# Performance work log

Measured on AMD Instinct MI355X. Metric: run time of the kernel, lower is better.

The kernel has to match this reference:

```python
import jax, jax.numpy as jnp
import numpy as np
import math

B, S, D, H, DFF = 2, 2048, 1024, 16, 4096
DK = D // H
LN_EPS = 1e-5


def setup_inputs() -> dict:
    key = jax.random.key(0)
    ks = jax.random.split(key, 16)
    s = 0.02
    inp = {
        "x": jax.random.normal(ks[0], (B, S, D), jnp.float32),
        "enc": jax.random.normal(ks[1], (B, S, D), jnp.float32),
        # causal mask for self-attention, full mask for cross-attention
        "tgt_mask": jnp.tril(jnp.ones((S, S), jnp.int32))[None, None, :, :],
        "src_mask": jnp.ones((1, 1, 1, S), jnp.int32),
        # self-attention projections (stored [in, out]; no bias)
        "sa_wq": jax.random.normal(ks[2], (D, D), jnp.float32) * s,
        "sa_wk": jax.random.normal(ks[3], (D, D), jnp.float32) * s,
        "sa_wv": jax.random.normal(ks[4], (D, D), jnp.float32) * s,
        "sa_wo": jax.random.normal(ks[5], (D, D), jnp.float32) * s,
        # cross-attention projections
        "ca_wq": jax.random.normal(ks[6], (D, D), jnp.float32) * s,
        "ca_wk": jax.random.normal(ks[7], (D, D), jnp.float32) * s,
        "ca_wv": jax.random.normal(ks[8], (D, D), jnp.float32) * s,
        "ca_wo": jax.random.normal(ks[9], (D, D), jnp.float32) * s,
        # feed-forward
        "ff_w1": jax.random.normal(ks[10], (D, DFF), jnp.float32) * s,
        "ff_b1": jnp.zeros((DFF,), jnp.float32),
        "ff_w2": jax.random.normal(ks[11], (DFF, D), jnp.float32) * s,
        "ff_b2": jnp.zeros((D,), jnp.float32),
        # layernorms (post-norm residuals)
        "ln1_g": jnp.ones((D,), jnp.float32), "ln1_b": jnp.zeros((D,), jnp.float32),
        "ln2_g": jnp.ones((D,), jnp.float32), "ln2_b": jnp.zeros((D,), jnp.float32),
        "ln3_g": jnp.ones((D,), jnp.float32), "ln3_b": jnp.zeros((D,), jnp.float32),
    }
    return inp


def _layernorm(x, g, b):
    mu = jnp.mean(x, axis=-1, keepdims=True)
    var = jnp.var(x, axis=-1, keepdims=True)
    return (x - mu) * jax.lax.rsqrt(var + LN_EPS) * g + b


def _mha(xq, xk, xv, wq, wk, wv, wo, mask):
    b, sq, d = xq.shape
    sk = xk.shape[1]
    Q = (xq @ wq).reshape(b, sq, H, DK).transpose(0, 2, 1, 3)  # [b,h,sq,dk]
    K = (xk @ wk).reshape(b, sk, H, DK).transpose(0, 2, 1, 3)
    V = (xv @ wv).reshape(b, sk, H, DK).transpose(0, 2, 1, 3)
    scores = jnp.einsum("bhqd,bhkd->bhqk", Q, K) / math.sqrt(DK)
    scores = jnp.where(mask == 0, -jnp.inf, scores)
    attn = jax.nn.softmax(scores, axis=-1)
    out = jnp.einsum("bhqk,bhkd->bhqd", attn, V)
    out = out.transpose(0, 2, 1, 3).reshape(b, sq, d)
    return out @ wo


def reference(x, enc, tgt_mask, src_mask,
              sa_wq, sa_wk, sa_wv, sa_wo,
              ca_wq, ca_wk, ca_wv, ca_wo,
              ff_w1, ff_b1, ff_w2, ff_b2,
              ln1_g, ln1_b, ln2_g, ln2_b, ln3_g, ln3_b):
    # self-attention + post-norm residual (dropout = 0)
    sa = _mha(x, x, x, sa_wq, sa_wk, sa_wv, sa_wo, tgt_mask)
    x = _layernorm(x + sa, ln1_g, ln1_b)
    # cross-attention + post-norm residual
    ca = _mha(x, enc, enc, ca_wq, ca_wk, ca_wv, ca_wo, src_mask)
    x = _layernorm(x + ca, ln2_g, ln2_b)
    # feed-forward + post-norm residual
    ff = jax.nn.relu(x @ ff_w1 + ff_b1) @ ff_w2 + ff_b2
    x = _layernorm(x + ff, ln3_g, ln3_b)
    return x
```

## Files before the change

kernel.cpp:

```cpp
#include <hip/hip_runtime.h>
#include <hip/hip_bf16.h>
#include <math.h>

#define Bc 2
#define Sc 2048
#define Dc 1024
#define Hc 16
#define DKc 64
#define DFFc 4096
#define Mrows (Bc * Sc)
#define LN_EPS 1e-5f

typedef __attribute__((ext_vector_type(8))) short short8;
typedef __attribute__((ext_vector_type(4))) float f32x4;
typedef unsigned short ushort_t;

__device__ __forceinline__ float bf2f(unsigned short u) {
  union { unsigned int i; float f; } v;
  v.i = ((unsigned int)u) << 16;
  return v.f;
}
__device__ __forceinline__ unsigned short f2bf(float f) {
  union { float f; unsigned int i; } v;
  v.f = f;
  unsigned int r = v.i + 0x7fffu + ((v.i >> 16) & 1u);
  return (unsigned short)(r >> 16);
}

__global__ __launch_bounds__(256) void cast_bf16_kernel(
    const float* __restrict__ in, ushort_t* __restrict__ out) {
  const int i = blockIdx.x * 256 + threadIdx.x;
  float4 v = reinterpret_cast<const float4*>(in)[i];
  ushort4 o;
  o.x = f2bf(v.x); o.y = f2bf(v.y); o.z = f2bf(v.z); o.w = f2bf(v.w);
  reinterpret_cast<ushort4*>(out)[i] = o;
}

__global__ __launch_bounds__(256) void transpose_cast_kernel(
    const float* __restrict__ W, ushort_t* __restrict__ Wt, int K, int N) {
  __shared__ float tile[32][33];
  const int t = threadIdx.x;
  const int k0 = blockIdx.y * 32, n0 = blockIdx.x * 32;
  const int r = t >> 3, c4 = (t & 7) * 4;
  float4 v = *reinterpret_cast<const float4*>(&W[(size_t)(k0 + r) * N + n0 + c4]);
  tile[r][c4 + 0] = v.x; tile[r][c4 + 1] = v.y;
  tile[r][c4 + 2] = v.z; tile[r][c4 + 3] = v.w;
  __syncthreads();
  ushort4 o;
  o.x = f2bf(tile[c4 + 0][r]);
  o.y = f2bf(tile[c4 + 1][r]);
  o.z = f2bf(tile[c4 + 2][r]);
  o.w = f2bf(tile[c4 + 3][r]);
  *reinterpret_cast<ushort4*>(&Wt[(size_t)(n0 + r) * K + k0 + c4]) = o;
}

template <int BM, bool BIAS, bool RELU, bool OBF16>
__global__ __launch_bounds__(256) void gemm_bf16_kernel(
    const ushort_t* __restrict__ A,
    const ushort_t* __restrict__ Bt,
    const float* __restrict__ bias,
    void* __restrict__ Cout, int M, int N, int K, float scale) {
  constexpr int MI = BM / 32;
  __shared__ __align__(16) ushort_t sA[BM * 32];
  __shared__ __align__(16) ushort_t sB[128 * 32];

  const int t = threadIdx.x;
  const int w = t >> 6;
  const int l = t & 63;
  const int wm = w >> 1, wn = w & 1;
  const int m0 = blockIdx.y * BM, n0 = blockIdx.x * 128;

  const int srow = t >> 2;
  const int scol = (t & 3) * 8;
  const ushort_t* gA = A + (size_t)(m0 + srow) * K + scol;
  const ushort_t* gB = Bt + (size_t)(n0 + srow) * K + scol;
  ushort_t* lA = sA + t * 8;
  ushort_t* lB = sB + t * 8;

  f32x4 acc[MI][4];
#pragma unroll
  for (int i = 0; i < MI; ++i)
#pragma unroll
    for (int j = 0; j < 4; ++j) acc[i][j] = (f32x4)0.f;

  const int fr = l & 15;
  const int fk = (l >> 4) * 8;

  for (int k0 = 0; k0 < K; k0 += 32) {
    __syncthreads();
    __builtin_amdgcn_global_load_lds(
        (const __attribute__((address_space(1))) void*)(gA),
        (__attribute__((address_space(3))) void*)(lA), 16, 0, 0);
    if constexpr (BM == 128)
      __builtin_amdgcn_global_load_lds(
          (const __attribute__((address_space(1))) void*)(gA + (size_t)64 * K),
          (__attribute__((address_space(3))) void*)(lA + 2048), 16, 0, 0);
    __builtin_amdgcn_global_load_lds(
        (const __attribute__((address_space(1))) void*)(gB),
        (__attribute__((address_space(3))) void*)(lB), 16, 0, 0);
    __builtin_amdgcn_global_load_lds(
        (const __attribute__((address_space(1))) void*)(gB + (size_t)64 * K),
        (__attribute__((address_space(3))) void*)(lB + 2048), 16, 0, 0);
    gA += 32;
    gB += 32;
    __syncthreads();

    short8 af[MI], bfr[4];
#pragma unroll
    for (int mi = 0; mi < MI; ++mi)
      af[mi] = *(const short8*)(sA + (wm * (16 * MI) + mi * 16 + fr) * 32 + fk);
#pragma unroll
    for (int ni = 0; ni < 4; ++ni)
      bfr[ni] = *(const short8*)(sB + (wn * 64 + ni * 16 + fr) * 32 + fk);
#pragma unroll
    for (int mi = 0; mi < MI; ++mi)
#pragma unroll
      for (int ni = 0; ni < 4; ++ni)
        acc[mi][ni] = __builtin_amdgcn_mfma_f32_16x16x32_bf16(
            af[mi], bfr[ni], acc[mi][ni], 0, 0, 0);
  }

  const int orow = (l >> 4) * 4;
  const int ocol = l & 15;
#pragma unroll
  for (int mi = 0; mi < MI; ++mi) {
#pragma unroll
    for (int ni = 0; ni < 4; ++ni) {
      const int gr = m0 + wm * (16 * MI) + mi * 16 + orow;
      const int gc = n0 + wn * 64 + ni * 16 + ocol;
      const float bv = BIAS ? bias[gc] : 0.f;
#pragma unroll
      for (int v = 0; v < 4; ++v) {
        float x = acc[mi][ni][v] * scale + bv;
        if (RELU) x = fmaxf(x, 0.f);
        if (OBF16)
          ((ushort_t*)Cout)[(size_t)(gr + v) * N + gc] = f2bf(x);
        else
          ((float*)Cout)[(size_t)(gr + v) * N + gc] = x;
      }
    }
  }
}

template <bool CAUSAL>
__global__ __launch_bounds__(256) void attn_mfma_kernel(
    const ushort_t* __restrict__ Q, const ushort_t* __restrict__ K,
    const ushort_t* __restrict__ Vt, ushort_t* __restrict__ O) {
  __shared__ __align__(16) ushort_t sK[64 * 64];
  __shared__ __align__(16) ushort_t sV[64 * 64];
  __shared__ __align__(16) ushort_t sP[4 * 16 * 64];

  const int t = threadIdx.x;
  const int w = t >> 6, l = t & 63;
  const int g = l >> 4, r = l & 15;
  const int q0 = blockIdx.x * 64;
  const int h = blockIdx.y, b = blockIdx.z;

  short8 qf[2];
  {
    const ushort_t* qp =
        Q + ((size_t)(b * Sc + q0 + w * 16 + r)) * Dc + h * DKc + g * 8;
    qf[0] = *(const short8*)(qp);
    qf[1] = *(const short8*)(qp + 32);
  }

  f32x4 oacc[4];
#pragma unroll
  for (int dt = 0; dt < 4; ++dt) oacc[dt] = (f32x4)0.f;
  float mrow = -1e30f, lrow = 0.f;

  const int i0 = t, i1 = 256 + t;
  const int r0 = i0 >> 3, c0 = ((i0 & 7) * 8) ^ ((r0 & 7) << 3);
  const int r1 = i1 >> 3, c1 = ((i1 & 7) * 8) ^ ((r1 & 7) << 3);
  const ushort_t* gK0 = K + ((size_t)(b * Sc) + r0) * Dc + h * DKc + c0;
  const ushort_t* gK1 = K + ((size_t)(b * Sc) + r1) * Dc + h * DKc + c1;
  const ushort_t* gV0 = Vt + ((size_t)(h * DKc) + r0) * Mrows + b * Sc + c0;
  const ushort_t* gV1 = Vt + ((size_t)(h * DKc) + r1) * Mrows + b * Sc + c1;
  ushort_t* lK0 = sK + i0 * 8;
  ushort_t* lK1 = sK + i1 * 8;
  ushort_t* lV0 = sV + i0 * 8;
  ushort_t* lV1 = sV + i1 * 8;

  ushort_t* pw = sP + w * 1024;
  const int swz = (r & 7) << 3;

  const int kt_last = CAUSAL ? (q0 >> 6) : (Sc / 64 - 1);
  for (int kt = 0; kt <= kt_last; ++kt) {
    const int k0 = kt * 64;
    __syncthreads();
    __builtin_amdgcn_global_load_lds(
        (const __attribute__((address_space(1))) void*)(gK0 + (size_t)k0 * Dc),
        (__attribute__((address_space(3))) void*)(lK0), 16, 0, 0);
    __builtin_amdgcn_global_load_lds(
        (const __attribute__((address_space(1))) void*)(gK1 + (size_t)k0 * Dc),
        (__attribute__((address_space(3))) void*)(lK1), 16, 0, 0);
    __builtin_amdgcn_global_load_lds(
        (const __attribute__((address_space(1))) void*)(gV0 + k0),
        (__attribute__((address_space(3))) void*)(lV0), 16, 0, 0);
    __builtin_amdgcn_global_load_lds(
        (const __attribute__((address_space(1))) void*)(gV1 + k0),
        (__attribute__((address_space(3))) void*)(lV1), 16, 0, 0);
    __syncthreads();

    f32x4 sacc[4];
#pragma unroll
    for (int nt = 0; nt < 4; ++nt) sacc[nt] = (f32x4)0.f;
#pragma unroll
    for (int ks = 0; ks < 2; ++ks) {
      const int dof = (ks * 32 + g * 8) ^ swz;
#pragma unroll
      for (int nt = 0; nt < 4; ++nt) {
        short8 kf = *(const short8*)(sK + (nt * 16 + r) * 64 + dof);
        sacc[nt] = __builtin_amdgcn_mfma_f32_16x16x32_bf16(kf, qf[ks],
                                                           sacc[nt], 0, 0, 0);
      }
    }

    const bool diag = CAUSAL && (kt == kt_last);
    float pmax = -1e30f;
#pragma unroll
    for (int nt = 0; nt < 4; ++nt)
#pragma unroll
      for (int v = 0; v < 4; ++v) {
        float s = sacc[nt][v];
        if (diag && (nt * 16 + g * 4 + v > w * 16 + r)) s = -1e30f;
        sacc[nt][v] = s;
        pmax = fmaxf(pmax, s);
      }
    pmax = fmaxf(pmax, __shfl_xor(pmax, 16));
    pmax = fmaxf(pmax, __shfl_xor(pmax, 32));
    const float mn = fmaxf(mrow, pmax);
    const float alpha = __expf(mrow - mn);
    mrow = mn;

    float psum = 0.f;
#pragma unroll
    for (int nt = 0; nt < 4; ++nt) {
      float p0 = __expf(sacc[nt][0] - mn);
      float p1 = __expf(sacc[nt][1] - mn);
      float p2 = __expf(sacc[nt][2] - mn);
      float p3 = __expf(sacc[nt][3] - mn);
      psum += (p0 + p1) + (p2 + p3);
      __hip_bfloat162 h01 = __float22bfloat162_rn(make_float2(p0, p1));
      __hip_bfloat162 h23 = __float22bfloat162_rn(make_float2(p2, p3));
      ushort_t* dst = pw + r * 64 + ((nt * 16 + g * 4) ^ swz);
      *reinterpret_cast<__hip_bfloat162*>(dst) = h01;
      *reinterpret_cast<__hip_bfloat162*>(dst + 2) = h23;
    }
    psum += __shfl_xor(psum, 16);
    psum += __shfl_xor(psum, 32);
    lrow = lrow * alpha + psum;
#pragma unroll
    for (int dt = 0; dt < 4; ++dt) oacc[dt] *= alpha;

#pragma unroll
    for (int ks = 0; ks < 2; ++ks) {
      const int kvo = (ks * 32 + g * 8) ^ swz;
      short8 pf = *(const short8*)(pw + r * 64 + kvo);
#pragma unroll
      for (int dt = 0; dt < 4; ++dt) {
        short8 vf = *(const short8*)(sV + (dt * 16 + r) * 64 + kvo);
        oacc[dt] = __builtin_amdgcn_mfma_f32_16x16x32_bf16(vf, pf,
                                                           oacc[dt], 0, 0, 0);
      }
    }
  }

  const float inv = 1.0f / lrow;
  ushort_t* ob =
      O + ((size_t)(b * Sc + q0 + w * 16 + r)) * Dc + h * DKc + g * 4;
#pragma unroll
  for (int dt = 0; dt < 4; ++dt) {
    ushort4 o4;
    o4.x = f2bf(oacc[dt][0] * inv);
    o4.y = f2bf(oacc[dt][1] * inv);
    o4.z = f2bf(oacc[dt][2] * inv);
    o4.w = f2bf(oacc[dt][3] * inv);
    *reinterpret_cast<ushort4*>(ob + dt * 16) = o4;
  }
}

template <bool WB>
__global__ __launch_bounds__(256) void add_ln_kernel(
    const float* __restrict__ X, const float* __restrict__ R,
    const float* __restrict__ g, const float* __restrict__ bta,
    float* __restrict__ out, ushort_t* __restrict__ outb) {
  const int row = blockIdx.x;
  const int t = threadIdx.x;
  const float4 xv = reinterpret_cast<const float4*>(X + (size_t)row * Dc)[t];
  const float4 rv = reinterpret_cast<const float4*>(R + (size_t)row * Dc)[t];
  float v[4] = {xv.x + rv.x, xv.y + rv.y, xv.z + rv.z, xv.w + rv.w};
  float s = v[0] + v[1] + v[2] + v[3];
  float ss = v[0] * v[0] + v[1] * v[1] + v[2] * v[2] + v[3] * v[3];
#pragma unroll
  for (int off = 32; off > 0; off >>= 1) {
    s += __shfl_down(s, off);
    ss += __shfl_down(ss, off);
  }
  __shared__ float sbuf[4], ssbuf[4];
  const int wid = t >> 6, lane = t & 63;
  if (lane == 0) { sbuf[wid] = s; ssbuf[wid] = ss; }
  __syncthreads();
  if (t == 0) {
    const float S1 = sbuf[0] + sbuf[1] + sbuf[2] + sbuf[3];
    const float S2 = ssbuf[0] + ssbuf[1] + ssbuf[2] + ssbuf[3];
    const float mu = S1 / Dc;
    const float var = S2 / Dc - mu * mu;
    sbuf[0] = mu;
    ssbuf[0] = rsqrtf(var + LN_EPS);
  }
  __syncthreads();
  const float mu = sbuf[0], rstd = ssbuf[0];
  const float4 gv = reinterpret_cast<const float4*>(g)[t];
  const float4 bv = reinterpret_cast<const float4*>(bta)[t];
  float4 o;
  o.x = (v[0] - mu) * rstd * gv.x + bv.x;
  o.y = (v[1] - mu) * rstd * gv.y + bv.y;
  o.z = (v[2] - mu) * rstd * gv.z + bv.z;
  o.w = (v[3] - mu) * rstd * gv.w + bv.w;
  reinterpret_cast<float4*>(out + (size_t)row * Dc)[t] = o;
  if (WB) {
    ushort4 ob;
    ob.x = f2bf(o.x); ob.y = f2bf(o.y); ob.z = f2bf(o.z); ob.w = f2bf(o.w);
    reinterpret_cast<ushort4*>(outb + (size_t)row * Dc)[t] = ob;
  }
}

template <int BM>
static inline void launch_gemm(const ushort_t* A, const ushort_t* Bt,
                               const float* bias, void* C, int M, int N, int K,
                               bool bias_on, bool relu_on, bool obf16,
                               float scale, hipStream_t stream) {
  dim3 grid(N / 128, M / BM);
  dim3 block(256);
  if (!bias_on && !relu_on && obf16)
    gemm_bf16_kernel<BM, false, false, true><<<grid, block, 0, stream>>>(
        A, Bt, bias, C, M, N, K, scale);
  else if (!bias_on && !relu_on && !obf16)
    gemm_bf16_kernel<BM, false, false, false><<<grid, block, 0, stream>>>(
        A, Bt, bias, C, M, N, K, scale);
  else if (bias_on && relu_on && obf16)
    gemm_bf16_kernel<BM, true, true, true><<<grid, block, 0, stream>>>(
        A, Bt, bias, C, M, N, K, scale);
  else
    gemm_bf16_kernel<BM, true, false, false><<<grid, block, 0, stream>>>(
        A, Bt, bias, C, M, N, K, scale);
}

extern "C" void kernel_launch(void* const* d_in, const int* in_sizes, int n_in,
                              void* d_out, int out_size, void* d_ws,
                              size_t ws_size, hipStream_t stream) {
  const float* x     = (const float*)d_in[0];
  const float* enc   = (const float*)d_in[1];
  const float* sa_wq = (const float*)d_in[4];
  const float* sa_wk = (const float*)d_in[5];
  const float* sa_wv = (const float*)d_in[6];
  const float* sa_wo = (const float*)d_in[7];
  const float* ca_wq = (const float*)d_in[8];
  const float* ca_wk = (const float*)d_in[9];
  const float* ca_wv = (const float*)d_in[10];
  const float* ca_wo = (const float*)d_in[11];
  const float* ff_w1 = (const float*)d_in[12];
  const float* ff_b1 = (const float*)d_in[13];
  const float* ff_w2 = (const float*)d_in[14];
  const float* ff_b2 = (const float*)d_in[15];
  const float* ln1_g = (const float*)d_in[16];
  const float* ln1_b = (const float*)d_in[17];
  const float* ln2_g = (const float*)d_in[18];
  const float* ln2_b = (const float*)d_in[19];
  const float* ln3_g = (const float*)d_in[20];
  const float* ln3_b = (const float*)d_in[21];

  const size_t MBf32 = (size_t)Mrows * Dc * 4;
  const size_t MBbf  = (size_t)Mrows * Dc * 2;
  const size_t W16   = 8 * (size_t)Dc * Dc * 2;
  const size_t need  = 2 * MBf32 + W16 + 6 * MBbf;
  if (ws_size < need) return;

  char* wsb = (char*)d_ws;
  float* xa = (float*)(wsb);
  float* Pb = (float*)(wsb + MBf32);
  ushort_t* wts = (ushort_t*)(wsb + 2 * MBf32);
  const size_t DD = (size_t)Dc * Dc;
  ushort_t* sa_wq_t = wts + 0 * DD;
  ushort_t* sa_wk_t = wts + 1 * DD;
  ushort_t* sa_wv_t = wts + 2 * DD;
  ushort_t* sa_wo_t = wts + 3 * DD;
  ushort_t* ca_wq_t = wts + 4 * DD;
  ushort_t* ca_wk_t = wts + 5 * DD;
  ushort_t* ca_wv_t = wts + 6 * DD;
  ushort_t* ca_wo_t = wts + 7 * DD;
  ushort_t* ff_w1_t = wts + 0 * DD;
  ushort_t* ff_w2_t = wts + 4 * DD;
  char* actb = wsb + 2 * MBf32 + W16;
  ushort_t* xb   = (ushort_t*)(actb);
  ushort_t* encb = (ushort_t*)(actb + 1 * MBbf);
  ushort_t* Qb   = (ushort_t*)(actb + 2 * MBbf);
  ushort_t* Kb   = (ushort_t*)(actb + 3 * MBbf);
  ushort_t* Vb   = (ushort_t*)(actb + 4 * MBbf);
  ushort_t* Tb   = (ushort_t*)(actb + 5 * MBbf);
  ushort_t* Fbb  = Qb;

  const int castGrid = Mrows * Dc / 4 / 256;
  dim3 tD(32, 32), tF1(DFFc / 32, Dc / 32), tF2(Dc / 32, DFFc / 32);
  dim3 attn_grid(Sc / 64, Hc, Bc);
  const float qs = 0.125f;

  cast_bf16_kernel<<<castGrid, 256, 0, stream>>>(x, xb);
  cast_bf16_kernel<<<castGrid, 256, 0, stream>>>(enc, encb);
  transpose_cast_kernel<<<tD, 256, 0, stream>>>(sa_wq, sa_wq_t, Dc, Dc);
  transpose_cast_kernel<<<tD, 256, 0, stream>>>(sa_wk, sa_wk_t, Dc, Dc);
  transpose_cast_kernel<<<tD, 256, 0, stream>>>(sa_wv, sa_wv_t, Dc, Dc);
  transpose_cast_kernel<<<tD, 256, 0, stream>>>(sa_wo, sa_wo_t, Dc, Dc);
  transpose_cast_kernel<<<tD, 256, 0, stream>>>(ca_wq, ca_wq_t, Dc, Dc);
  transpose_cast_kernel<<<tD, 256, 0, stream>>>(ca_wk, ca_wk_t, Dc, Dc);
  transpose_cast_kernel<<<tD, 256, 0, stream>>>(ca_wv, ca_wv_t, Dc, Dc);
  transpose_cast_kernel<<<tD, 256, 0, stream>>>(ca_wo, ca_wo_t, Dc, Dc);

  launch_gemm<64>(xb, sa_wq_t, nullptr, Qb, Mrows, Dc, Dc, false, false, true, qs, stream);
  launch_gemm<64>(xb, sa_wk_t, nullptr, Kb, Mrows, Dc, Dc, false, false, true, 1.f, stream);
  launch_gemm<64>(sa_wv_t, xb, nullptr, Vb, Dc, Mrows, Dc, false, false, true, 1.f, stream);
  attn_mfma_kernel<true><<<attn_grid, 256, 0, stream>>>(Qb, Kb, Vb, Tb);
  launch_gemm<64>(Tb, sa_wo_t, nullptr, Pb, Mrows, Dc, Dc, false, false, false, 1.f, stream);
  add_ln_kernel<true><<<Mrows, 256, 0, stream>>>(x, Pb, ln1_g, ln1_b, xa, xb);

  launch_gemm<64>(xb, ca_wq_t, nullptr, Qb, Mrows, Dc, Dc, false, false, true, qs, stream);
  launch_gemm<64>(encb, ca_wk_t, nullptr, Kb, Mrows, Dc, Dc, false, false, true, 1.f, stream);
  launch_gemm<64>(ca_wv_t, encb, nullptr, Vb, Dc, Mrows, Dc, false, false, true, 1.f, stream);
  attn_mfma_kernel<false><<<attn_grid, 256, 0, stream>>>(Qb, Kb, Vb, Tb);
  launch_gemm<64>(Tb, ca_wo_t, nullptr, Pb, Mrows, Dc, Dc, false, false, false, 1.f, stream);
  add_ln_kernel<true><<<Mrows, 256, 0, stream>>>(xa, Pb, ln2_g, ln2_b, xa, xb);

  transpose_cast_kernel<<<tF1, 256, 0, stream>>>(ff_w1, ff_w1_t, Dc, DFFc);
  transpose_cast_kernel<<<tF2, 256, 0, stream>>>(ff_w2, ff_w2_t, DFFc, Dc);
  launch_gemm<128>(xb, ff_w1_t, ff_b1, Fbb, Mrows, DFFc, Dc, true, true, true, 1.f, stream);
  launch_gemm<64>(Fbb, ff_w2_t, ff_b2, Pb, Mrows, Dc, DFFc, true, false, false, 1.f, stream);
  add_ln_kernel<false><<<Mrows, 256, 0, stream>>>(xa, Pb, ln3_g, ln3_b,
                                                  (float*)d_out, nullptr);
}
```

Baseline: 664.3 us.

## Fuse Q/K projection GEMM, batch weight transposes, swizzle LDS and remap blocks

Merges the self-attention Q and K projections into one GEMM with N=2048 by relying on sa_wq_t and sa_wk_t being adjacent in memory, and applies the softmax scale only to the first 1024 columns. The attention kernel takes row strides so it can read Q and K from the interleaved output. The eight weight transpose-casts become one launch with a z-dimension, cutting launch overhead. The GEMM gets an XOR swizzle on LDS columns to reduce bank conflicts, and both GEMM and attention remap block IDs across XCDs for better cache locality. The swizzle relies on the direct global-to-LDS load addressing matching the fragment-read XOR pattern.

```diff
diff --git a/kernel.cpp b/kernel.cpp
--- a/kernel.cpp
+++ b/kernel.cpp
@@ -54,12 +54,33 @@
   *reinterpret_cast<ushort4*>(&Wt[(size_t)(n0 + r) * K + k0 + c4]) = o;
 }
 
+struct TC8 { const float* src[8]; ushort_t* dst[8]; };
+__global__ __launch_bounds__(256) void transpose_cast8_kernel(TC8 p) {
+  __shared__ float tile[32][33];
+  const float* W = p.src[blockIdx.z];
+  ushort_t* Wt = p.dst[blockIdx.z];
+  const int t = threadIdx.x;
+  const int k0 = blockIdx.y * 32, n0 = blockIdx.x * 32;
+  const int r = t >> 3, c4 = (t & 7) * 4;
+  float4 v = *reinterpret_cast<const float4*>(&W[(size_t)(k0 + r) * Dc + n0 + c4]);
+  tile[r][c4 + 0] = v.x; tile[r][c4 + 1] = v.y;
+  tile[r][c4 + 2] = v.z; tile[r][c4 + 3] = v.w;
+  __syncthreads();
+  ushort4 o;
+  o.x = f2bf(tile[c4 + 0][r]);
+  o.y = f2bf(tile[c4 + 1][r]);
+  o.z = f2bf(tile[c4 + 2][r]);
+  o.w = f2bf(tile[c4 + 3][r]);
+  *reinterpret_cast<ushort4*>(&Wt[(size_t)(n0 + r) * Dc + k0 + c4]) = o;
+}
+
 template <int BM, bool BIAS, bool RELU, bool OBF16>
 __global__ __launch_bounds__(256) void gemm_bf16_kernel(
     const ushort_t* __restrict__ A,
     const ushort_t* __restrict__ Bt,
     const float* __restrict__ bias,
-    void* __restrict__ Cout, int M, int N, int K, float scale) {
+    void* __restrict__ Cout, int M, int N, int K,
+    float scale, int scale_ncols) {
   constexpr int MI = BM / 32;
   __shared__ __align__(16) ushort_t sA[BM * 32];
   __shared__ __align__(16) ushort_t sB[128 * 32];
@@ -68,10 +89,15 @@
   const int w = t >> 6;
   const int l = t & 63;
   const int wm = w >> 1, wn = w & 1;
-  const int m0 = blockIdx.y * BM, n0 = blockIdx.x * 128;
+
+  const int nwg = gridDim.x * gridDim.y;
+  int lid = blockIdx.y * gridDim.x + blockIdx.x;
+  lid = (lid & 7) * (nwg >> 3) + (lid >> 3);
+  const int m0 = (lid / gridDim.x) * BM;
+  const int n0 = (lid % gridDim.x) * 128;
 
   const int srow = t >> 2;
-  const int scol = (t & 3) * 8;
+  const int scol = (((t & 3) ^ (srow & 3)) * 8);
   const ushort_t* gA = A + (size_t)(m0 + srow) * K + scol;
   const ushort_t* gB = Bt + (size_t)(n0 + srow) * K + scol;
   ushort_t* lA = sA + t * 8;
@@ -84,7 +110,7 @@
     for (int j = 0; j < 4; ++j) acc[i][j] = (f32x4)0.f;
 
   const int fr = l & 15;
-  const int fk = (l >> 4) * 8;
+  const int fk = (((l >> 4) ^ (l & 3)) * 8);
 
   for (int k0 = 0; k0 < K; k0 += 32) {
     __syncthreads();
@@ -128,10 +154,11 @@
     for (int ni = 0; ni < 4; ++ni) {
       const int gr = m0 + wm * (16 * MI) + mi * 16 + orow;
       const int gc = n0 + wn * 64 + ni * 16 + ocol;
+      const float sc = (gc < scale_ncols) ? scale : 1.0f;
       const float bv = BIAS ? bias[gc] : 0.f;
 #pragma unroll
       for (int v = 0; v < 4; ++v) {
-        float x = acc[mi][ni][v] * scale + bv;
+        float x = acc[mi][ni][v] * sc + bv;
         if (RELU) x = fmaxf(x, 0.f);
         if (OBF16)
           ((ushort_t*)Cout)[(size_t)(gr + v) * N + gc] = f2bf(x);
@@ -145,7 +172,8 @@
 template <bool CAUSAL>
 __global__ __launch_bounds__(256) void attn_mfma_kernel(
     const ushort_t* __restrict__ Q, const ushort_t* __restrict__ K,
-    const ushort_t* __restrict__ Vt, ushort_t* __restrict__ O) {
+    const ushort_t* __restrict__ Vt, ushort_t* __restrict__ O,
+    int qstride, int kstride) {
   __shared__ __align__(16) ushort_t sK[64 * 64];
   __shared__ __align__(16) ushort_t sV[64 * 64];
   __shared__ __align__(16) ushort_t sP[4 * 16 * 64];
@@ -153,13 +181,18 @@
   const int t = threadIdx.x;
   const int w = t >> 6, l = t & 63;
   const int g = l >> 4, r = l & 15;
-  const int q0 = blockIdx.x * 64;
-  const int h = blockIdx.y, b = blockIdx.z;
+
+  const int nwg = gridDim.x * gridDim.y * gridDim.z;
+  int f = (blockIdx.z * gridDim.y + blockIdx.y) * gridDim.x + blockIdx.x;
+  f = (f & 7) * (nwg >> 3) + (f >> 3);
+  const int q0 = (f % gridDim.x) * 64;
+  const int h = (f / gridDim.x) % gridDim.y;
+  const int b = f / (gridDim.x * gridDim.y);
 
   short8 qf[2];
   {
     const ushort_t* qp =
-        Q + ((size_t)(b * Sc + q0 + w * 16 + r)) * Dc + h * DKc + g * 8;
+        Q + ((size_t)(b * Sc + q0 + w * 16 + r)) * qstride + h * DKc + g * 8;
     qf[0] = *(const short8*)(qp);
     qf[1] = *(const short8*)(qp + 32);
   }
@@ -172,8 +205,8 @@
   const int i0 = t, i1 = 256 + t;
   const int r0 = i0 >> 3, c0 = ((i0 & 7) * 8) ^ ((r0 & 7) << 3);
   const int r1 = i1 >> 3, c1 = ((i1 & 7) * 8) ^ ((r1 & 7) << 3);
-  const ushort_t* gK0 = K + ((size_t)(b * Sc) + r0) * Dc + h * DKc + c0;
-  const ushort_t* gK1 = K + ((size_t)(b * Sc) + r1) * Dc + h * DKc + c1;
+  const ushort_t* gK0 = K + ((size_t)(b * Sc) + r0) * kstride + h * DKc + c0;
+  const ushort_t* gK1 = K + ((size_t)(b * Sc) + r1) * kstride + h * DKc + c1;
   const ushort_t* gV0 = Vt + ((size_t)(h * DKc) + r0) * Mrows + b * Sc + c0;
   const ushort_t* gV1 = Vt + ((size_t)(h * DKc) + r1) * Mrows + b * Sc + c1;
   ushort_t* lK0 = sK + i0 * 8;
@@ -189,10 +222,10 @@
     const int k0 = kt * 64;
     __syncthreads();
     __builtin_amdgcn_global_load_lds(
-        (const __attribute__((address_space(1))) void*)(gK0 + (size_t)k0 * Dc),
+        (const __attribute__((address_space(1))) void*)(gK0 + (size_t)k0 * kstride),
         (__attribute__((address_space(3))) void*)(lK0), 16, 0, 0);
     __builtin_amdgcn_global_load_lds(
-        (const __attribute__((address_space(1))) void*)(gK1 + (size_t)k0 * Dc),
+        (const __attribute__((address_space(1))) void*)(gK1 + (size_t)k0 * kstride),
         (__attribute__((address_space(3))) void*)(lK1), 16, 0, 0);
     __builtin_amdgcn_global_load_lds(
         (const __attribute__((address_space(1))) void*)(gV0 + k0),
@@ -330,21 +363,22 @@
 static inline void launch_gemm(const ushort_t* A, const ushort_t* Bt,
                                const float* bias, void* C, int M, int N, int K,
                                bool bias_on, bool relu_on, bool obf16,
-                               float scale, hipStream_t stream) {
+                               float scale, int scale_ncols,
+                               hipStream_t stream) {
   dim3 grid(N / 128, M / BM);
   dim3 block(256);
   if (!bias_on && !relu_on && obf16)
     gemm_bf16_kernel<BM, false, false, true><<<grid, block, 0, stream>>>(
-        A, Bt, bias, C, M, N, K, scale);
+        A, Bt, bias, C, M, N, K, scale, scale_ncols);
   else if (!bias_on && !relu_on && !obf16)
     gemm_bf16_kernel<BM, false, false, false><<<grid, block, 0, stream>>>(
-        A, Bt, bias, C, M, N, K, scale);
+        A, Bt, bias, C, M, N, K, scale, scale_ncols);
   else if (bias_on && relu_on && obf16)
     gemm_bf16_kernel<BM, true, true, true><<<grid, block, 0, stream>>>(
-        A, Bt, bias, C, M, N, K, scale);
+        A, Bt, bias, C, M, N, K, scale, scale_ncols);
   else
     gemm_bf16_kernel<BM, true, false, false><<<grid, block, 0, stream>>>(
-        A, Bt, bias, C, M, N, K, scale);
+        A, Bt, bias, C, M, N, K, scale, scale_ncols);
 }
 
 extern "C" void kernel_launch(void* const* d_in, const int* in_sizes, int n_in,
@@ -402,39 +436,51 @@
   ushort_t* Fbb  = Qb;
 
   const int castGrid = Mrows * Dc / 4 / 256;
-  dim3 tD(32, 32), tF1(DFFc / 32, Dc / 32), tF2(Dc / 32, DFFc / 32);
+  dim3 t8(32, 32, 8), tF1(DFFc / 32, Dc / 32), tF2(Dc / 32, DFFc / 32);
   dim3 attn_grid(Sc / 64, Hc, Bc);
   const float qs = 0.125f;
 
   cast_bf16_kernel<<<castGrid, 256, 0, stream>>>(x, xb);
   cast_bf16_kernel<<<castGrid, 256, 0, stream>>>(enc, encb);
-  transpose_cast_kernel<<<tD, 256, 0, stream>>>(sa_wq, sa_wq_t, Dc, Dc);
-  transpose_cast_kernel<<<tD, 256, 0, stream>>>(sa_wk, sa_wk_t, Dc, Dc);
-  transpose_cast_kernel<<<tD, 256, 0, stream>>>(sa_wv, sa_wv_t, Dc, Dc);
-  transpose_cast_kernel<<<tD, 256, 0, stream>>>(sa_wo, sa_wo_t, Dc, Dc);
-  transpose_cast_kernel<<<tD, 256, 0, stream>>>(ca_wq, ca_wq_t, Dc, Dc);
-  transpose_cast_kernel<<<tD, 256, 0, stream>>>(ca_wk, ca_wk_t, Dc, Dc);
-  transpose_cast_kernel<<<tD, 256, 0, stream>>>(ca_wv, ca_wv_t, Dc, Dc);
-  transpose_cast_kernel<<<tD, 256, 0, stream>>>(ca_wo, ca_wo_t, Dc, Dc);
-
-  launch_gemm<64>(xb, sa_wq_t, nullptr, Qb, Mrows, Dc, Dc, false, false, true, qs, stream);
-  launch_gemm<64>(xb, sa_wk_t, nullptr, Kb, Mrows, Dc, Dc, false, false, true, 1.f, stream);
-  launch_gemm<64>(sa_wv_t, xb, nullptr, Vb, Dc, Mrows, Dc, false, false, true, 1.f, stream);
-  attn_mfma_kernel<true><<<attn_grid, 256, 0, stream>>>(Qb, Kb, Vb, Tb);
-  launch_gemm<64>(Tb, sa_wo_t, nullptr, Pb, Mrows, Dc, Dc, false, false, false, 1.f, stream);
+  TC8 tc;
+  tc.src[0] = sa_wq; tc.dst[0] = sa_wq_t;
+  tc.src[1] = sa_wk; tc.dst[1] = sa_wk_t;
+  tc.src[2] = sa_wv; tc.dst[2] = sa_wv_t;
+  tc.src[3] = sa_wo; tc.dst[3] = sa_wo_t;
+  tc.src[4] = ca_wq; tc.dst[4] = ca_wq_t;
+  tc.src[5] = ca_wk; tc.dst[5] = ca_wk_t;
+  tc.src[6] = ca_wv; tc.dst[6] = ca_wv_t;
+  tc.src[7] = ca_wo; tc.dst[7] = ca_wo_t;
+  transpose_cast8_kernel<<<t8, 256, 0, stream>>>(tc);
+
+  launch_gemm<64>(xb, sa_wq_t, nullptr, Qb, Mrows, 2048, Dc,
+                  false, false, true, qs, 1024, stream);
+  launch_gemm<64>(sa_wv_t, xb, nullptr, Vb, Dc, Mrows, Dc,
+                  false, false, true, 1.f, 0, stream);
+  attn_mfma_kernel<true><<<attn_grid, 256, 0, stream>>>(
+      Qb, Qb + 1024, Vb, Tb, 2048, 2048);
+  launch_gemm<64>(Tb, sa_wo_t, nullptr, Pb, Mrows, Dc, Dc,
+                  false, false, false, 1.f, 0, stream);
   add_ln_kernel<true><<<Mrows, 256, 0, stream>>>(x, Pb, ln1_g, ln1_b, xa, xb);
 
-  launch_gemm<64>(xb, ca_wq_t, nullptr, Qb, Mrows, Dc, Dc, false, false, true, qs, stream);
-  launch_gemm<64>(encb, ca_wk_t, nullptr, Kb, Mrows, Dc, Dc, false, false, true, 1.f, stream);
-  launch_gemm<64>(ca_wv_t, encb, nullptr, Vb, Dc, Mrows, Dc, false, false, true, 1.f, stream);
-  attn_mfma_kernel<false><<<attn_grid, 256, 0, stream>>>(Qb, Kb, Vb, Tb);
-  launch_gemm<64>(Tb, ca_wo_t, nullptr, Pb, Mrows, Dc, Dc, false, false, false, 1.f, stream);
+  launch_gemm<64>(xb, ca_wq_t, nullptr, Qb, Mrows, Dc, Dc,
+                  false, false, true, qs, 1024, stream);
+  launch_gemm<64>(encb, ca_wk_t, nullptr, Kb, Mrows, Dc, Dc,
+                  false, false, true, 1.f, 0, stream);
+  launch_gemm<64>(ca_wv_t, encb, nullptr, Vb, Dc, Mrows, Dc,
+                  false, false, true, 1.f, 0, stream);
+  attn_mfma_kernel<false><<<attn_grid, 256, 0, stream>>>(
+      Qb, Kb, Vb, Tb, 1024, 1024);
+  launch_gemm<64>(Tb, ca_wo_t, nullptr, Pb, Mrows, Dc, Dc,
+                  false, false, false, 1.f, 0, stream);
   add_ln_kernel<true><<<Mrows, 256, 0, stream>>>(xa, Pb, ln2_g, ln2_b, xa, xb);
 
   transpose_cast_kernel<<<tF1, 256, 0, stream>>>(ff_w1, ff_w1_t, Dc, DFFc);
   transpose_cast_kernel<<<tF2, 256, 0, stream>>>(ff_w2, ff_w2_t, DFFc, Dc);
-  launch_gemm<128>(xb, ff_w1_t, ff_b1, Fbb, Mrows, DFFc, Dc, true, true, true, 1.f, stream);
-  launch_gemm<64>(Fbb, ff_w2_t, ff_b2, Pb, Mrows, Dc, DFFc, true, false, false, 1.f, stream);
+  launch_gemm<128>(xb, ff_w1_t, ff_b1, Fbb, Mrows, DFFc, Dc,
+                   true, true, true, 1.f, 0, stream);
+  launch_gemm<64>(Fbb, ff_w2_t, ff_b2, Pb, Mrows, Dc, DFFc,
+                  true, false, false, 1.f, 0, stream);
   add_ln_kernel<false><<<Mrows, 256, 0, stream>>>(xa, Pb, ln3_g, ln3_b,
                                                   (float*)d_out, nullptr);
 }
```

Result: faster. 618.0 us (-7.0%).
